# Performance work log

Measured on AMD Instinct MI355X. Metric: run time of the kernel, lower is better.

## Reference

```python
import jax, jax.numpy as jnp
import numpy as np

HID = 768
HEADS = 12
HEAD_LEN = HID // HEADS
SCALE_INV = 1.0 / np.sqrt(HEAD_LEN).astype(np.float32)


def setup_inputs() -> dict:
    key = jax.random.key(0)
    ks = jax.random.split(key, 5)
    std = 1.0 / np.sqrt(HID)
    return {
        "x": jax.random.normal(ks[0], (1, 4096, HID), dtype=jnp.float32),
        "w_q": jax.random.normal(ks[1], (HID, HID), dtype=jnp.float32) * std,
        "w_k": jax.random.normal(ks[2], (HID, HID), dtype=jnp.float32) * std,
        "w_v": jax.random.normal(ks[3], (HID, HID), dtype=jnp.float32) * std,
        "w_fc": jax.random.normal(ks[4], (HID, HID), dtype=jnp.float32) * std,
    }


def reference(x, w_q, w_k, w_v, w_fc):
    B, S, D = x.shape
    # torch Linear weight layout [out, in]: y = x @ W.T
    def proj_heads(w):
        y = jnp.einsum("bsd,ed->bse", x, w)
        return y.reshape(B, S, HEADS, HEAD_LEN).transpose(0, 2, 1, 3)  # bhsd
    q = proj_heads(w_q)
    k = proj_heads(w_k)
    v = proj_heads(w_v)
    scores = SCALE_INV * jnp.einsum("bhqd,bhkd->bhqk", q, k)
    attn = jax.nn.softmax(scores, axis=-1)
    out = jnp.einsum("bhqk,bhkd->bhqd", attn, v)
    out = out.transpose(0, 2, 1, 3).reshape(B, S, D)
    return jnp.einsum("bsd,ed->bse", out, w_fc)
```

## Files before the change

kernel.cpp:

```cpp
#include <hip/hip_runtime.h>
#include <hip/hip_bf16.h>

#define S_LEN 4096
#define HID 768
#define NHEAD 12
#define HL 64
#define PSS 72
#define QB 64

typedef __attribute__((ext_vector_type(8))) short short8;
typedef __attribute__((ext_vector_type(4))) float f32x4;
using bf16 = __hip_bfloat16;

__device__ __forceinline__ void gl2lds16(const void* g, void* l) {
  __builtin_amdgcn_global_load_lds((__attribute__((address_space(1))) void*)(g),
                                   (__attribute__((address_space(3))) void*)(l),
                                   16, 0, 0);
}

__device__ __forceinline__ f32x4 mfma_bf16(short8 a, short8 b, f32x4 c) {
  return __builtin_amdgcn_mfma_f32_16x16x32_bf16(a, b, c, 0, 0, 0);
}

__device__ __forceinline__ void storeC(float* C, long idx, float v) { C[idx] = v; }
__device__ __forceinline__ void storeC(bf16* C, long idx, float v) { C[idx] = __float2bfloat16(v); }

#define BAR() asm volatile("s_waitcnt lgkmcnt(0)\n\ts_barrier" ::: "memory")

__global__ __launch_bounds__(256) void cvt_all(
    const float* __restrict__ x, const float* __restrict__ wq,
    const float* __restrict__ wk, const float* __restrict__ wv,
    const float* __restrict__ wfc, bf16* __restrict__ xb, bf16* __restrict__ wqb,
    bf16* __restrict__ wkb, bf16* __restrict__ wvb, bf16* __restrict__ wfcb) {
  const long NX = (long)S_LEN * HID;
  const long NW = (long)HID * HID;
  long i = ((long)blockIdx.x * 256 + threadIdx.x) * 4;
  const float* src;
  bf16* dst;
  long off;
  if (i < NX) {
    src = x; dst = xb; off = i;
  } else {
    long j = i - NX;
    int wsel = (int)(j / NW);
    off = j - (long)wsel * NW;
    src = wsel == 0 ? wq : wsel == 1 ? wk : wsel == 2 ? wv : wfc;
    dst = wsel == 0 ? wqb : wsel == 1 ? wkb : wsel == 2 ? wvb : wfcb;
  }
  float4 v = *(const float4*)(src + off);
  bf16 h0 = __float2bfloat16(v.x), h1 = __float2bfloat16(v.y);
  bf16 h2 = __float2bfloat16(v.z), h3 = __float2bfloat16(v.w);
  ushort4 o;
  o.x = *(unsigned short*)&h0; o.y = *(unsigned short*)&h1;
  o.z = *(unsigned short*)&h2; o.w = *(unsigned short*)&h3;
  *(ushort4*)(dst + off) = o;
}

template <typename OT>
__global__ __launch_bounds__(256) void gemm_bt(
    const bf16* __restrict__ A, const bf16* __restrict__ B0,
    const bf16* __restrict__ B1, const bf16* __restrict__ B2,
    OT* __restrict__ C0, OT* __restrict__ C1, OT* __restrict__ C2, float qscale) {
  constexpr int K = HID;
  __shared__ __align__(16) bf16 As[128 * 32];
  __shared__ __align__(16) bf16 Bs[128 * 32];
  const int z = blockIdx.z;
  const bf16* B = (z == 0) ? B0 : (z == 1) ? B1 : B2;
  OT* C = (z == 0) ? C0 : (z == 1) ? C1 : C2;
  const float sc = (z == 0) ? qscale : 1.0f;
  const int bm = blockIdx.y, bn = blockIdx.x;
  const int t = threadIdx.x, lane = t & 63, w = t >> 6;
  const int wm = w >> 1, wn = w & 1;
  const int q4 = lane >> 4, c16 = lane & 15;
  const int srow = lane >> 2, scol = (lane & 3) * 8;
  const bf16* Ab = A + (long)bm * 128 * K;
  const bf16* Bb = B + (long)bn * 128 * K;
  f32x4 acc[4][4] = {};
  for (int k0 = 0; k0 < K; k0 += 32) {
#pragma unroll
    for (int r = 0; r < 2; ++r) {
      int rowb = r * 64 + w * 16;
      gl2lds16(Ab + (long)(rowb + srow) * K + k0 + scol, &As[rowb * 32]);
      gl2lds16(Bb + (long)(rowb + srow) * K + k0 + scol, &Bs[rowb * 32]);
    }
    __syncthreads();
    short8 af[4], bfv[4];
#pragma unroll
    for (int i = 0; i < 4; ++i)
      af[i] = *(const short8*)&As[(wm * 64 + i * 16 + c16) * 32 + q4 * 8];
#pragma unroll
    for (int j = 0; j < 4; ++j)
      bfv[j] = *(const short8*)&Bs[(wn * 64 + j * 16 + c16) * 32 + q4 * 8];
#pragma unroll
    for (int i = 0; i < 4; ++i)
#pragma unroll
      for (int j = 0; j < 4; ++j)
        acc[i][j] = mfma_bf16(af[i], bfv[j], acc[i][j]);
    __syncthreads();
  }
  const long crow0 = (long)bm * 128 + wm * 64;
  const int ccol0 = bn * 128 + wn * 64;
#pragma unroll
  for (int i = 0; i < 4; ++i)
#pragma unroll
    for (int j = 0; j < 4; ++j)
#pragma unroll
      for (int r = 0; r < 4; ++r) {
        long row = crow0 + i * 16 + q4 * 4 + r;
        int col = ccol0 + j * 16 + c16;
        storeC(C, row * HID + col, sc * acc[i][j][r]);
      }
}

__global__ __launch_bounds__(256) void gemm_fc(const bf16* __restrict__ A,
                                               const bf16* __restrict__ B,
                                               float* __restrict__ C) {
  __shared__ __align__(16) bf16 As[128 * 32];
  __shared__ __align__(16) bf16 Bs[64 * 32];
  const int bm = blockIdx.y, bn = blockIdx.x;
  const int t = threadIdx.x, lane = t & 63, w = t >> 6;
  const int q4 = lane >> 4, c16 = lane & 15;
  const int srow = lane >> 2, scol = (lane & 3) * 8;
  const bf16* Ab = A + (long)bm * 128 * HID;
  const bf16* Bb = B + (long)bn * 64 * HID;
  f32x4 acc[2][4] = {};
  for (int k0 = 0; k0 < HID; k0 += 32) {
#pragma unroll
    for (int r = 0; r < 2; ++r) {
      int rowb = w * 32 + r * 16;
      gl2lds16(Ab + (long)(rowb + srow) * HID + k0 + scol, &As[rowb * 32]);
    }
    gl2lds16(Bb + (long)(w * 16 + srow) * HID + k0 + scol, &Bs[w * 16 * 32]);
    __syncthreads();
    short8 af[2], bfv[4];
#pragma unroll
    for (int i = 0; i < 2; ++i)
      af[i] = *(const short8*)&As[(w * 32 + i * 16 + c16) * 32 + q4 * 8];
#pragma unroll
    for (int j = 0; j < 4; ++j)
      bfv[j] = *(const short8*)&Bs[(j * 16 + c16) * 32 + q4 * 8];
#pragma unroll
    for (int i = 0; i < 2; ++i)
#pragma unroll
      for (int j = 0; j < 4; ++j)
        acc[i][j] = mfma_bf16(af[i], bfv[j], acc[i][j]);
    __syncthreads();
  }
#pragma unroll
  for (int i = 0; i < 2; ++i)
#pragma unroll
    for (int j = 0; j < 4; ++j)
#pragma unroll
      for (int r = 0; r < 4; ++r) {
        long row = (long)bm * 128 + w * 32 + i * 16 + q4 * 4 + r;
        int col = bn * 64 + j * 16 + c16;
        C[row * HID + col] = acc[i][j][r];
      }
}

__global__ __launch_bounds__(256) void transpose_v(const bf16* __restrict__ V,
                                                   bf16* __restrict__ Vt) {
  __shared__ unsigned short tile[64][65];
  const int bs = blockIdx.x * 64;
  const int be = blockIdx.y * 64;
  const int t = threadIdx.x;
#pragma unroll
  for (int p = 0; p < 4; ++p) {
    int i = p * 256 + t;
    int r = i >> 4;
    int c = (i & 15) * 4;
    ushort4 v = *(const ushort4*)((const unsigned short*)V + (long)(bs + r) * HID + be + c);
    tile[r][c] = v.x; tile[r][c + 1] = v.y; tile[r][c + 2] = v.z; tile[r][c + 3] = v.w;
  }
  __syncthreads();
#pragma unroll
  for (int p = 0; p < 4; ++p) {
    int i = p * 256 + t;
    int r = i >> 4;
    int c = (i & 15) * 4;
    ushort4 v;
    v.x = tile[c][r]; v.y = tile[c + 1][r]; v.z = tile[c + 2][r]; v.w = tile[c + 3][r];
    *(ushort4*)((unsigned short*)Vt + (long)(be + r) * S_LEN + bs + c) = v;
  }
}

__global__ __launch_bounds__(256, 3) void flash_attn(const bf16* __restrict__ Q,
                                                     const bf16* __restrict__ Kg,
                                                     const bf16* __restrict__ Vt,
                                                     bf16* __restrict__ O) {
  __shared__ __align__(16) bf16 Ps[2][QB * PSS];
  __shared__ float Lred[4][QB];
  const int i = blockIdx.x;
  const int xcd = i & 7, s = i >> 3;
  const int pair = xcd >> 1;
  const int r2 = s * 2 + (xcd & 1);
  const int h = pair * 3 + (r2 >> 6);
  const int qt = r2 & 63;
  const int t = threadIdx.x, lane = t & 63, w = t >> 6;
  const int q4 = lane >> 4, c16 = lane & 15;
  const int s0 = qt * QB;

  short8 qf[2][4];
  {
    const bf16* Qb = Q + (long)(s0 + c16) * HID + h * HL + q4 * 8;
#pragma unroll
    for (int j = 0; j < 4; ++j)
#pragma unroll
      for (int ks = 0; ks < 2; ++ks)
        qf[ks][j] = *(const short8*)(Qb + (long)j * 16 * HID + ks * 32);
  }
  const bf16* kp = Kg + (long)(w * 16 + c16) * HID + h * HL + q4 * 8;
  const bf16* vp = Vt + (long)(h * HL + w * 16 + c16) * S_LEN + q4 * 8;

  float l_part[4] = {0.f, 0.f, 0.f, 0.f};
  f32x4 o_acc[4] = {};

  short8 kf0 = *(const short8*)(kp), kf1 = *(const short8*)(kp + 32);
  short8 vf0 = *(const short8*)(vp), vf1 = *(const short8*)(vp + 32);

  {
    f32x4 sacc[4] = {};
#pragma unroll
    for (int j = 0; j < 4; ++j) sacc[j] = mfma_bf16(kf0, qf[0][j], sacc[j]);
#pragma unroll
    for (int j = 0; j < 4; ++j) sacc[j] = mfma_bf16(kf1, qf[1][j], sacc[j]);
    kp += 64 * HID;
    kf0 = *(const short8*)(kp); kf1 = *(const short8*)(kp + 32);
#pragma unroll
    for (int j = 0; j < 4; ++j) {
      float p0 = __builtin_amdgcn_exp2f(sacc[j][0]);
      float p1 = __builtin_amdgcn_exp2f(sacc[j][1]);
      float p2 = __builtin_amdgcn_exp2f(sacc[j][2]);
      float p3 = __builtin_amdgcn_exp2f(sacc[j][3]);
      l_part[j] += (p0 + p1) + (p2 + p3);
      bf16 b0 = __float2bfloat16(p0), b1 = __float2bfloat16(p1);
      bf16 b2 = __float2bfloat16(p2), b3 = __float2bfloat16(p3);
      short4 pk;
      pk.x = *(short*)&b0; pk.y = *(short*)&b1; pk.z = *(short*)&b2; pk.w = *(short*)&b3;
      *(short4*)&Ps[0][(j * 16 + c16) * PSS + w * 16 + q4 * 4] = pk;
    }
  }
  BAR();

  constexpr int NT = S_LEN / 64;
  for (int kt = 0; kt < NT - 1; ++kt) {
    const int cur = kt & 1, nxt = cur ^ 1;
    const bf16* kpn = (kt + 2 < NT) ? kp + 64 * HID : kp;
    const bf16* vpn = vp + 64;
    short8 nk0 = *(const short8*)(kpn), nk1 = *(const short8*)(kpn + 32);
    short8 nv0 = *(const short8*)(vpn), nv1 = *(const short8*)(vpn + 32);

    f32x4 sacc[4] = {};
#pragma unroll
    for (int j = 0; j < 4; ++j) sacc[j] = mfma_bf16(kf0, qf[0][j], sacc[j]);
#pragma unroll
    for (int j = 0; j < 4; ++j) sacc[j] = mfma_bf16(kf1, qf[1][j], sacc[j]);

#pragma unroll
    for (int ks = 0; ks < 2; ++ks) {
      short8 vfk = ks ? vf1 : vf0;
#pragma unroll
      for (int j = 0; j < 4; ++j) {
        short8 pf = *(const short8*)&Ps[cur][(j * 16 + c16) * PSS + ks * 32 + q4 * 8];
        o_acc[j] = mfma_bf16(vfk, pf, o_acc[j]);
      }
    }

#pragma unroll
    for (int j = 0; j < 4; ++j) {
      float p0 = __builtin_amdgcn_exp2f(sacc[j][0]);
      float p1 = __builtin_amdgcn_exp2f(sacc[j][1]);
      float p2 = __builtin_amdgcn_exp2f(sacc[j][2]);
      float p3 = __builtin_amdgcn_exp2f(sacc[j][3]);
      l_part[j] += (p0 + p1) + (p2 + p3);
      bf16 b0 = __float2bfloat16(p0), b1 = __float2bfloat16(p1);
      bf16 b2 = __float2bfloat16(p2), b3 = __float2bfloat16(p3);
      short4 pk;
      pk.x = *(short*)&b0; pk.y = *(short*)&b1; pk.z = *(short*)&b2; pk.w = *(short*)&b3;
      *(short4*)&Ps[nxt][(j * 16 + c16) * PSS + w * 16 + q4 * 4] = pk;
    }

    BAR();
    kf0 = nk0; kf1 = nk1; vf0 = nv0; vf1 = nv1;
    kp = kpn; vp = vpn;
  }

  {
    const int cur = (NT - 1) & 1;
#pragma unroll
    for (int ks = 0; ks < 2; ++ks) {
      short8 vfk = ks ? vf1 : vf0;
#pragma unroll
      for (int j = 0; j < 4; ++j) {
        short8 pf = *(const short8*)&Ps[cur][(j * 16 + c16) * PSS + ks * 32 + q4 * 8];
        o_acc[j] = mfma_bf16(vfk, pf, o_acc[j]);
      }
    }
  }

#pragma unroll
  for (int j = 0; j < 4; ++j) {
    float s = l_part[j];
    s += __shfl_xor(s, 16, 64);
    s += __shfl_xor(s, 32, 64);
    Lred[w][j * 16 + c16] = s;
  }
  BAR();
#pragma unroll
  for (int j = 0; j < 4; ++j) {
    int q = j * 16 + c16;
    float lt = Lred[0][q] + Lred[1][q] + Lred[2][q] + Lred[3][q];
    float rl = 1.0f / lt;
    float v0 = o_acc[j][0] * rl, v1 = o_acc[j][1] * rl;
    float v2 = o_acc[j][2] * rl, v3 = o_acc[j][3] * rl;
    bf16 b0 = __float2bfloat16(v0), b1 = __float2bfloat16(v1);
    bf16 b2 = __float2bfloat16(v2), b3 = __float2bfloat16(v3);
    short4 pk;
    pk.x = *(short*)&b0; pk.y = *(short*)&b1; pk.z = *(short*)&b2; pk.w = *(short*)&b3;
    *(short4*)&O[(long)(s0 + q) * HID + h * HL + w * 16 + q4 * 4] = pk;
  }
}

extern "C" void kernel_launch(void* const* d_in, const int* in_sizes, int n_in,
                              void* d_out, int out_size, void* d_ws, size_t ws_size,
                              hipStream_t stream) {
  const float* x = (const float*)d_in[0];
  const float* wq = (const float*)d_in[1];
  const float* wk = (const float*)d_in[2];
  const float* wv = (const float*)d_in[3];
  const float* wfc = (const float*)d_in[4];
  float* out = (float*)d_out;

  const long NBIG = (long)S_LEN * HID * sizeof(bf16);
  const long NWB = (long)HID * HID * sizeof(bf16);
  char* p = (char*)d_ws;
  bf16* xb = (bf16*)p;   p += NBIG;
  bf16* wqb = (bf16*)p;  p += NWB;
  bf16* wkb = (bf16*)p;  p += NWB;
  bf16* wvb = (bf16*)p;  p += NWB;
  bf16* wfcb = (bf16*)p; p += NWB;
  bf16* Qb = (bf16*)p;   p += NBIG;
  bf16* Kb = (bf16*)p;   p += NBIG;
  bf16* Vb = (bf16*)p;   p += NBIG;
  bf16* Vtb = (bf16*)p;  p += NBIG;
  bf16* Ob = (bf16*)p;   p += NBIG;

  const float c1 = 0.125f * 1.44269504088896340736f;

  const long total4 = ((long)S_LEN * HID + 4L * HID * HID) / 4;
  cvt_all<<<(int)(total4 / 256), 256, 0, stream>>>(x, wq, wk, wv, wfc, xb, wqb, wkb,
                                                   wvb, wfcb);
  gemm_bt<bf16><<<dim3(HID / 128, S_LEN / 128, 3), 256, 0, stream>>>(
      xb, wqb, wkb, wvb, Qb, Kb, Vb, c1);
  transpose_v<<<dim3(S_LEN / 64, HID / 64), 256, 0, stream>>>(Vb, Vtb);
  flash_attn<<<dim3(S_LEN / QB * NHEAD), 256, 0, stream>>>(Qb, Kb, Vtb, Ob);
  gemm_fc<<<dim3(HID / 64, S_LEN / 128), 256, 0, stream>>>(Ob, wfcb, out);
}
```

Baseline: 211.6 us.

## Split key range across two wave groups per attention block and merge partials

The flash attention kernel now launches 512 threads per block. Two groups of four waves each process half of the key/value sequence, with separate double-buffered P tiles in shared memory. At the end, group 1 writes its partial output accumulators into shared memory that aliases the P buffers. Group 0 adds them in, sums all eight row-sum partials, normalises and stores the result. This shortens each block's serial key loop and gives each CU more waves to hide latency, at the cost of an extra shared-memory reduction, barriers across eight waves, and tighter register limits from the new launch bounds.

```diff
diff --git a/kernel.cpp b/kernel.cpp
--- a/kernel.cpp
+++ b/kernel.cpp
@@ -7,6 +7,7 @@
 #define HL 64
 #define PSS 72
 #define QB 64
+#define ORST 68
 
 typedef __attribute__((ext_vector_type(8))) short short8;
 typedef __attribute__((ext_vector_type(4))) float f32x4;
@@ -184,21 +185,24 @@
   }
 }
 
-__global__ __launch_bounds__(256, 3) void flash_attn(const bf16* __restrict__ Q,
+__global__ __launch_bounds__(512, 6) void flash_attn(const bf16* __restrict__ Q,
                                                      const bf16* __restrict__ Kg,
                                                      const bf16* __restrict__ Vt,
                                                      bf16* __restrict__ O) {
-  __shared__ __align__(16) bf16 Ps[2][QB * PSS];
-  __shared__ float Lred[4][QB];
-  const int i = blockIdx.x;
-  const int xcd = i & 7, s = i >> 3;
+  __shared__ __align__(16) bf16 PsBuf[2][2][QB * PSS];
+  __shared__ float Lred[8][QB];
+  float* Mred = (float*)&PsBuf[0][0][0];
+  const int i0 = blockIdx.x;
+  const int xcd = i0 & 7, sb = i0 >> 3;
   const int pair = xcd >> 1;
-  const int r2 = s * 2 + (xcd & 1);
+  const int r2 = sb * 2 + (xcd & 1);
   const int h = pair * 3 + (r2 >> 6);
   const int qt = r2 & 63;
   const int t = threadIdx.x, lane = t & 63, w = t >> 6;
+  const int g = w >> 2, wg = w & 3;
   const int q4 = lane >> 4, c16 = lane & 15;
   const int s0 = qt * QB;
+  constexpr int NTH = S_LEN / 64 / 2;
 
   short8 qf[2][4];
   {
@@ -209,11 +213,14 @@
       for (int ks = 0; ks < 2; ++ks)
         qf[ks][j] = *(const short8*)(Qb + (long)j * 16 * HID + ks * 32);
   }
-  const bf16* kp = Kg + (long)(w * 16 + c16) * HID + h * HL + q4 * 8;
-  const bf16* vp = Vt + (long)(h * HL + w * 16 + c16) * S_LEN + q4 * 8;
+  const bf16* kp = Kg + (long)(g * NTH * 64 + wg * 16 + c16) * HID + h * HL + q4 * 8;
+  const bf16* vp = Vt + (long)(h * HL + wg * 16 + c16) * S_LEN + g * NTH * 64 + q4 * 8;
 
   float l_part[4] = {0.f, 0.f, 0.f, 0.f};
   f32x4 o_acc[4] = {};
+
+  bf16* psG0 = &PsBuf[g][0][0];
+  bf16* psG1 = &PsBuf[g][1][0];
 
   short8 kf0 = *(const short8*)(kp), kf1 = *(const short8*)(kp + 32);
   short8 vf0 = *(const short8*)(vp), vf1 = *(const short8*)(vp + 32);
@@ -237,15 +244,15 @@
       bf16 b2 = __float2bfloat16(p2), b3 = __float2bfloat16(p3);
       short4 pk;
       pk.x = *(short*)&b0; pk.y = *(short*)&b1; pk.z = *(short*)&b2; pk.w = *(short*)&b3;
-      *(short4*)&Ps[0][(j * 16 + c16) * PSS + w * 16 + q4 * 4] = pk;
+      *(short4*)&psG0[(j * 16 + c16) * PSS + wg * 16 + q4 * 4] = pk;
     }
   }
   BAR();
 
-  constexpr int NT = S_LEN / 64;
-  for (int kt = 0; kt < NT - 1; ++kt) {
-    const int cur = kt & 1, nxt = cur ^ 1;
-    const bf16* kpn = (kt + 2 < NT) ? kp + 64 * HID : kp;
+  for (int tau = 0; tau < NTH - 1; ++tau) {
+    bf16* psCur = (tau & 1) ? psG1 : psG0;
+    bf16* psNxt = (tau & 1) ? psG0 : psG1;
+    const bf16* kpn = (tau + 2 < NTH) ? kp + 64 * HID : kp;
     const bf16* vpn = vp + 64;
     short8 nk0 = *(const short8*)(kpn), nk1 = *(const short8*)(kpn + 32);
     short8 nv0 = *(const short8*)(vpn), nv1 = *(const short8*)(vpn + 32);
@@ -261,7 +268,7 @@
       short8 vfk = ks ? vf1 : vf0;
 #pragma unroll
       for (int j = 0; j < 4; ++j) {
-        short8 pf = *(const short8*)&Ps[cur][(j * 16 + c16) * PSS + ks * 32 + q4 * 8];
+        short8 pf = *(const short8*)&psCur[(j * 16 + c16) * PSS + ks * 32 + q4 * 8];
         o_acc[j] = mfma_bf16(vfk, pf, o_acc[j]);
       }
     }
@@ -277,7 +284,7 @@
       bf16 b2 = __float2bfloat16(p2), b3 = __float2bfloat16(p3);
       short4 pk;
       pk.x = *(short*)&b0; pk.y = *(short*)&b1; pk.z = *(short*)&b2; pk.w = *(short*)&b3;
-      *(short4*)&Ps[nxt][(j * 16 + c16) * PSS + w * 16 + q4 * 4] = pk;
+      *(short4*)&psNxt[(j * 16 + c16) * PSS + wg * 16 + q4 * 4] = pk;
     }
 
     BAR();
@@ -286,13 +293,13 @@
   }
 
   {
-    const int cur = (NT - 1) & 1;
+    bf16* psCur = ((NTH - 1) & 1) ? psG1 : psG0;
 #pragma unroll
     for (int ks = 0; ks < 2; ++ks) {
       short8 vfk = ks ? vf1 : vf0;
 #pragma unroll
       for (int j = 0; j < 4; ++j) {
-        short8 pf = *(const short8*)&Ps[cur][(j * 16 + c16) * PSS + ks * 32 + q4 * 8];
+        short8 pf = *(const short8*)&psCur[(j * 16 + c16) * PSS + ks * 32 + q4 * 8];
         o_acc[j] = mfma_bf16(vfk, pf, o_acc[j]);
       }
     }
@@ -305,19 +312,33 @@
     s += __shfl_xor(s, 32, 64);
     Lred[w][j * 16 + c16] = s;
   }
-  BAR();
-#pragma unroll
-  for (int j = 0; j < 4; ++j) {
-    int q = j * 16 + c16;
-    float lt = Lred[0][q] + Lred[1][q] + Lred[2][q] + Lred[3][q];
-    float rl = 1.0f / lt;
-    float v0 = o_acc[j][0] * rl, v1 = o_acc[j][1] * rl;
-    float v2 = o_acc[j][2] * rl, v3 = o_acc[j][3] * rl;
-    bf16 b0 = __float2bfloat16(v0), b1 = __float2bfloat16(v1);
-    bf16 b2 = __float2bfloat16(v2), b3 = __float2bfloat16(v3);
-    short4 pk;
-    pk.x = *(short*)&b0; pk.y = *(short*)&b1; pk.z = *(short*)&b2; pk.w = *(short*)&b3;
-    *(short4*)&O[(long)(s0 + q) * HID + h * HL + w * 16 + q4 * 4] = pk;
+  __syncthreads();
+
+  if (g == 1) {
+#pragma unroll
+    for (int j = 0; j < 4; ++j)
+#pragma unroll
+      for (int r = 0; r < 4; ++r)
+        Mred[(wg * 16 + q4 * 4 + r) * ORST + j * 16 + c16] = o_acc[j][r];
+  }
+  __syncthreads();
+  if (g == 0) {
+#pragma unroll
+    for (int j = 0; j < 4; ++j) {
+      int q = j * 16 + c16;
+      float lt = ((Lred[0][q] + Lred[1][q]) + (Lred[2][q] + Lred[3][q])) +
+                 ((Lred[4][q] + Lred[5][q]) + (Lred[6][q] + Lred[7][q]));
+      float rl = 1.0f / lt;
+      float v0 = (o_acc[j][0] + Mred[(wg * 16 + q4 * 4 + 0) * ORST + q]) * rl;
+      float v1 = (o_acc[j][1] + Mred[(wg * 16 + q4 * 4 + 1) * ORST + q]) * rl;
+      float v2 = (o_acc[j][2] + Mred[(wg * 16 + q4 * 4 + 2) * ORST + q]) * rl;
+      float v3 = (o_acc[j][3] + Mred[(wg * 16 + q4 * 4 + 3) * ORST + q]) * rl;
+      bf16 b0 = __float2bfloat16(v0), b1 = __float2bfloat16(v1);
+      bf16 b2 = __float2bfloat16(v2), b3 = __float2bfloat16(v3);
+      short4 pk;
+      pk.x = *(short*)&b0; pk.y = *(short*)&b1; pk.z = *(short*)&b2; pk.w = *(short*)&b3;
+      *(short4*)&O[(long)(s0 + q) * HID + h * HL + wg * 16 + q4 * 4] = pk;
+    }
   }
 }
 
@@ -353,6 +374,6 @@
   gemm_bt<bf16><<<dim3(HID / 128, S_LEN / 128, 3), 256, 0, stream>>>(
       xb, wqb, wkb, wvb, Qb, Kb, Vb, c1);
   transpose_v<<<dim3(S_LEN / 64, HID / 64), 256, 0, stream>>>(Vb, Vtb);
-  flash_attn<<<dim3(S_LEN / QB * NHEAD), 256, 0, stream>>>(Qb, Kb, Vtb, Ob);
+  flash_attn<<<dim3(S_LEN / QB * NHEAD), 512, 0, stream>>>(Qb, Kb, Vtb, Ob);
   gemm_fc<<<dim3(HID / 64, S_LEN / 128), 256, 0, stream>>>(Ob, wfcb, out);
 }
```

Result: slower. 281.2 us (+32.9%).
